# Optimization experiments

Measured on AMD Instinct MI355X. Metric: run time of the kernel, lower is better.

## Reference

```python
import jax, jax.numpy as jnp
import numpy as np

N = 10000       # num_nodes
E = 1000        # num_hyperedges
STEPS = 30      # horizon


def setup_inputs() -> dict:
    key = jax.random.key(0)
    k1, k2 = jax.random.split(key, 2)
    infected0 = jax.random.uniform(k1, (N,)) < 0.01
    x = jnp.stack([(~infected0).astype(jnp.float32),
                   infected0.astype(jnp.float32),
                   jnp.zeros((N,), jnp.float32)], axis=1)
    H = (jax.random.uniform(k2, (STEPS - 1, E, N)) < 0.001).astype(jnp.float32)
    beta = jnp.full((N,), 0.01, jnp.float32)
    gamma = jnp.full((N,), 0.038, jnp.float32)
    return {"x": x, "H": H, "beta": beta, "gamma": gamma, "steps": STEPS}


def _simulate(x, H, beta, gamma):
    n = x.shape[0]
    key0 = jax.random.key(42)

    def step(carry, H_t):
        p_prev, s_prev, key = carry
        key, k1, k2 = jax.random.split(key, 3)
        infected = s_prev[:, 1]
        # hypergraph Laplacian step: H_t.T @ (H_t @ infected)
        new_cases = beta * (H_t.T @ (H_t @ infected))
        new_rec = gamma * infected
        p = jnp.stack([p_prev[:, 0] - new_cases,
                       p_prev[:, 1] + new_cases - new_rec,
                       p_prev[:, 2] + new_rec], axis=1)
        p = jnp.clip(p, 0.0, 1.0)
        # per-node stochastic SIR state transitions (vectorized)
        u1 = jax.random.uniform(k1, (n,))
        u2 = jax.random.uniform(k2, (n,))
        was_S = s_prev[:, 0] == 1
        was_I = s_prev[:, 1] == 1
        s_to_I = was_S & (u1 < p[:, 1])
        i_event = was_I & (u1 < p[:, 2])
        i_to_R = i_event & (u2 < 0.5)
        i_to_S = i_event & ~(u2 < 0.5)
        new_S = (was_S & ~s_to_I) | i_to_S
        new_I = s_to_I | (was_I & ~i_event)
        new_R = (~was_S & ~was_I) | i_to_R
        s = jnp.stack([new_S, new_I, new_R], axis=1).astype(x.dtype)
        return (p, s, key), (p, s)

    (_, _, _), (p_seq, s_seq) = jax.lax.scan(step, (x, x, key0), H)
    pathogen = jnp.concatenate([x[None], p_seq], axis=0)    # (steps, N, 3)
    state = jnp.concatenate([x[None], s_seq], axis=0)       # (steps, N, 3)
    return pathogen, state


def reference(x, H, beta, gamma, steps):
    # steps == H.shape[0] + 1 by construction
    return _simulate(x, H, beta, gamma)
```

## Files before the change

kernel.cpp:

```cpp
#include <hip/hip_runtime.h>
#include <stdint.h>

constexpr int NN = 10000;
constexpr int EE = 1000;
constexpr int TT = 30;
constexpr int TS = TT - 1;
constexpr int ROW = NN * 3;
constexpr int S_OFF = TT * ROW;
constexpr int CAP_E = 48;
constexpr int WPR = CAP_E / 2;
constexpr int PREW = 8;
constexpr int SIMT = 1024;
constexpr int NPT  = 10;
constexpr int RBLK = (NN + SIMT - 1) / SIMT;

__host__ __device__ inline void tf2x32(uint32_t k0, uint32_t k1,
                                       uint32_t x0, uint32_t x1,
                                       uint32_t &o0, uint32_t &o1) {
  uint32_t ks2 = k0 ^ k1 ^ 0x1BD11BDAu;
  x0 += k0; x1 += k1;
#define TFR(r) do { x0 += x1; x1 = (x1 << (r)) | (x1 >> (32 - (r))); x1 ^= x0; } while (0)
  TFR(13); TFR(15); TFR(26); TFR(6);
  x0 += k1;  x1 += ks2 + 1u;
  TFR(17); TFR(29); TFR(16); TFR(24);
  x0 += ks2; x1 += k0 + 2u;
  TFR(13); TFR(15); TFR(26); TFR(6);
  x0 += k0;  x1 += k1 + 3u;
  TFR(17); TFR(29); TFR(16); TFR(24);
  x0 += k1;  x1 += ks2 + 4u;
  TFR(13); TFR(15); TFR(26); TFR(6);
  x0 += ks2; x1 += k0 + 5u;
#undef TFR
  o0 = x0; o1 = x1;
}

__device__ inline float bits_to_uniform(uint32_t bits) {
  float f = __uint_as_float((bits >> 9) | 0x3F800000u) - 1.0f;
  return f < 0.f ? 0.f : f;
}

struct StepKeys { uint32_t k1a[TS], k1b[TS], k2a[TS], k2b[TS]; };

__device__ inline void bar_lds() {
  asm volatile("s_waitcnt lgkmcnt(0)\n\ts_barrier" ::: "memory");
}

#define ALD(p)    __hip_atomic_load((p),  __ATOMIC_RELAXED, __HIP_MEMORY_SCOPE_AGENT)
#define AST(p, v) __hip_atomic_store((p), (v), __ATOMIC_RELAXED, __HIP_MEMORY_SCOPE_AGENT)

__global__ void k_zero(unsigned* __restrict__ cnt) {
  if (threadIdx.x < TS) cnt[threadIdx.x] = 0u;
}

__global__ __launch_bounds__(SIMT, 4)
void k_fused(const float* __restrict__ H,
             int* __restrict__ edge_cnt, uint32_t* __restrict__ edge_words,
             unsigned long long* __restrict__ uv, unsigned* __restrict__ cnt,
             const float* __restrict__ x,
             const float* __restrict__ beta, const float* __restrict__ gamma_,
             float* __restrict__ out, StepKeys keys) {
  const int tid = threadIdx.x;

  if (blockIdx.x > 0) {
    const int row = blockIdx.x - 1;
    const int t = row / EE;
    const int e = row - t * EE;

    if (e < RBLK) {
      int n = e * SIMT + tid;
      if (n < NN) {
        uint32_t a, b;
        tf2x32(keys.k1a[t], keys.k1b[t], 0u, (uint32_t)n, a, b);
        uint32_t b1 = __float_as_uint(bits_to_uniform(a ^ b));
        tf2x32(keys.k2a[t], keys.k2b[t], 0u, (uint32_t)n, a, b);
        uint32_t b2 = __float_as_uint(bits_to_uniform(a ^ b));
        unsigned long long raw = (unsigned long long)b1 | ((unsigned long long)b2 << 32);
        AST(&uv[(size_t)t * NN + n], raw);
      }
    }

    __shared__ int scnt;
    __shared__ uint16_t list[CAP_E];
    if (tid == 0) scnt = 0;
    __syncthreads();
    const float4* hrow = reinterpret_cast<const float4*>(H + (size_t)row * NN);
    float4 v0 = hrow[tid];
    float4 v1 = hrow[tid + 1024];
    float4 v2 = make_float4(0.f, 0.f, 0.f, 0.f);
    const bool has2 = tid + 2048 < NN / 4;
    if (has2) v2 = hrow[tid + 2048];
#define PROC(v, b4) do { \
    if ((v).x != 0.f) { int p = atomicAdd(&scnt, 1); if (p < CAP_E) list[p] = (uint16_t)((b4) + 0); } \
    if ((v).y != 0.f) { int p = atomicAdd(&scnt, 1); if (p < CAP_E) list[p] = (uint16_t)((b4) + 1); } \
    if ((v).z != 0.f) { int p = atomicAdd(&scnt, 1); if (p < CAP_E) list[p] = (uint16_t)((b4) + 2); } \
    if ((v).w != 0.f) { int p = atomicAdd(&scnt, 1); if (p < CAP_E) list[p] = (uint16_t)((b4) + 3); } \
  } while (0)
    PROC(v0, 4 * tid);
    PROC(v1, 4 * (tid + 1024));
    if (has2) PROC(v2, 4 * (tid + 2048));
#undef PROC
    __syncthreads();
    int c = scnt < CAP_E ? scnt : CAP_E;
    if (tid == 0) AST(&edge_cnt[row], c);
    int words = (c + 1) >> 1;
    int wmax = words > PREW ? words : PREW;
    if (tid < wmax) {
      uint32_t lo = (2 * tid     < c) ? (uint32_t)list[2 * tid]     : 0xFFFFu;
      uint32_t hi = (2 * tid + 1 < c) ? (uint32_t)list[2 * tid + 1] : 0xFFFFu;
      AST(&edge_words[((size_t)t * WPR + tid) * EE + e], lo | (hi << 16));
    }
    __syncthreads();
    if (tid == 0)
      __hip_atomic_fetch_add(&cnt[t], 1u, __ATOMIC_RELAXED, __HIP_MEMORY_SCOPE_AGENT);
    return;
  }

  __shared__ int nvst[NN];

  float p0[NPT], p1[NPT], p2[NPT], bet[NPT], gam[NPT];
#pragma unroll
  for (int k = 0; k < NPT; ++k) {
    int n = tid + k * SIMT;
    if (n < NN) {
      float x0 = x[n * 3 + 0], x1 = x[n * 3 + 1], x2 = x[n * 3 + 2];
      p0[k] = x0; p1[k] = x1; p2[k] = x2;
      int st = (x1 == 1.f) ? 1 : ((x0 == 1.f) ? 0 : 2);
      nvst[n] = st << 16;
      bet[k] = beta[n]; gam[k] = gamma_[n];
      out[n * 3 + 0] = x0; out[n * 3 + 1] = x1; out[n * 3 + 2] = x2;
      out[S_OFF + n * 3 + 0] = x0; out[S_OFF + n * 3 + 1] = x1; out[S_OFF + n * 3 + 2] = x2;
    }
  }
  bar_lds();

  for (int t = 0; t < TS; ++t) {
    if (tid == 0) {
      while (ALD(&cnt[t]) < (unsigned)EE) __builtin_amdgcn_s_sleep(8);
    }
    bar_lds();

    float u1r[NPT], u2r[NPT];
#pragma unroll
    for (int k = 0; k < NPT; ++k) {
      int n = tid + k * SIMT;
      if (n < NN) {
        unsigned long long raw = ALD(&uv[(size_t)t * NN + n]);
        u1r[k] = __uint_as_float((uint32_t)raw);
        u2r[k] = __uint_as_float((uint32_t)(raw >> 32));
      }
    }

    if (tid < EE) {
      const uint32_t* wb = edge_words + (size_t)t * WPR * EE + tid;
      int ec = ALD(&edge_cnt[t * EE + tid]); if (ec > CAP_E) ec = CAP_E;
      uint32_t w[PREW];
#pragma unroll
      for (int j = 0; j < PREW; ++j) w[j] = ALD(&wb[(size_t)j * EE]);
      int words = (ec + 1) >> 1;
      int s = 0;
#pragma unroll
      for (int j = 0; j < PREW; ++j) {
        uint32_t lo = w[j] & 0xFFFFu, hi = w[j] >> 16;
        if (lo != 0xFFFFu) s += ((nvst[lo] >> 16) == 1) ? 1 : 0;
        if (hi != 0xFFFFu) s += ((nvst[hi] >> 16) == 1) ? 1 : 0;
      }
      for (int j = PREW; j < words; ++j) {
        uint32_t ww = ALD(&wb[(size_t)j * EE]);
        uint32_t lo = ww & 0xFFFFu, hi = ww >> 16;
        if (lo != 0xFFFFu) s += ((nvst[lo] >> 16) == 1) ? 1 : 0;
        if (hi != 0xFFFFu) s += ((nvst[hi] >> 16) == 1) ? 1 : 0;
      }
      if (s > 0) {
#pragma unroll
        for (int j = 0; j < PREW; ++j) {
          uint32_t lo = w[j] & 0xFFFFu, hi = w[j] >> 16;
          if (lo != 0xFFFFu) atomicAdd(&nvst[lo], s);
          if (hi != 0xFFFFu) atomicAdd(&nvst[hi], s);
        }
        for (int j = PREW; j < words; ++j) {
          uint32_t ww = ALD(&wb[(size_t)j * EE]);
          uint32_t lo = ww & 0xFFFFu, hi = ww >> 16;
          if (lo != 0xFFFFu) atomicAdd(&nvst[lo], s);
          if (hi != 0xFFFFu) atomicAdd(&nvst[hi], s);
        }
      }
    }
    bar_lds();

    float* po = out + (size_t)(t + 1) * ROW;
    float* so = out + S_OFF + (size_t)(t + 1) * ROW;
#pragma unroll
    for (int k = 0; k < NPT; ++k) {
      int n = tid + k * SIMT;
      if (n < NN) {
        int wv = nvst[n];
        int v  = wv & 0xFFFF;
        int st = wv >> 16;
        float s1 = (st == 1) ? 1.f : 0.f;
        float new_cases = __fmul_rn(bet[k], (float)v);
        float new_rec   = __fmul_rn(gam[k], s1);
        float q0 = fminf(1.f, fmaxf(0.f, __fsub_rn(p0[k], new_cases)));
        float q1 = fminf(1.f, fmaxf(0.f, __fsub_rn(__fadd_rn(p1[k], new_cases), new_rec)));
        float q2 = fminf(1.f, fmaxf(0.f, __fadd_rn(p2[k], new_rec)));
        p0[k] = q0; p1[k] = q1; p2[k] = q2;

        bool was_S  = (st == 0);
        bool was_I  = (st == 1);
        bool s_to_I = was_S && (u1r[k] < q1);
        bool i_event = was_I && (u1r[k] < q2);
        bool u2lt   = (u2r[k] < 0.5f);
        bool i_to_R = i_event && u2lt;
        bool i_to_S = i_event && !u2lt;
        bool new_S = (was_S && !s_to_I) || i_to_S;
        bool new_I = s_to_I || (was_I && !i_event);
        bool new_R = (!was_S && !was_I) || i_to_R;

        po[n * 3 + 0] = q0; po[n * 3 + 1] = q1; po[n * 3 + 2] = q2;
        so[n * 3 + 0] = new_S ? 1.f : 0.f;
        so[n * 3 + 1] = new_I ? 1.f : 0.f;
        so[n * 3 + 2] = new_R ? 1.f : 0.f;
        nvst[n] = (new_I ? 1 : (new_S ? 0 : 2)) << 16;
      }
    }
  }
}

extern "C" void kernel_launch(void* const* d_in, const int* in_sizes, int n_in,
                              void* d_out, int out_size, void* d_ws, size_t ws_size,
                              hipStream_t stream) {
  const float* x      = (const float*)d_in[0];
  const float* H      = (const float*)d_in[1];
  const float* beta   = (const float*)d_in[2];
  const float* gamma_ = (const float*)d_in[3];
  float* out = (float*)d_out;

  StepKeys keys;
  uint32_t key0 = 0u, key1 = 42u;
  for (int t = 0; t < TS; ++t) {
    uint32_t a0, b0, a1, b1, a2, b2;
    tf2x32(key0, key1, 0u, 0u, a0, b0);
    tf2x32(key0, key1, 0u, 1u, a1, b1);
    tf2x32(key0, key1, 0u, 2u, a2, b2);
    keys.k1a[t] = a1; keys.k1b[t] = b1; keys.k2a[t] = a2; keys.k2b[t] = b2;
    key0 = a0; key1 = b0;
  }

  size_t off = 0;
  auto take = [&](size_t bytes) { size_t o = off; off += (bytes + 255) & ~(size_t)255; return o; };
  size_t o_ec = take((size_t)TS * EE * sizeof(int));
  size_t o_ew = take((size_t)TS * WPR * EE * sizeof(uint32_t));
  size_t o_uv = take((size_t)TS * NN * sizeof(unsigned long long));
  size_t o_ct = take((size_t)TS * sizeof(unsigned));

  int*      edge_cnt   = (int*)((char*)d_ws + o_ec);
  uint32_t* edge_words = (uint32_t*)((char*)d_ws + o_ew);
  unsigned long long* uv = (unsigned long long*)((char*)d_ws + o_uv);
  unsigned* cnt        = (unsigned*)((char*)d_ws + o_ct);

  k_zero<<<1, 64, 0, stream>>>(cnt);
  k_fused<<<1 + TS * EE, SIMT, 0, stream>>>(H, edge_cnt, edge_words, uv, cnt,
                                            x, beta, gamma_, out, keys);
}
```

Baseline: 1.608 ms.

## Process five incidence rows per producer block with upfront batched loads

Each producer block now handles five consecutive hyperedge rows of the same timestep instead of one. All five rows of H are loaded into registers before processing, which raises memory-level parallelism. It also cuts the block count and the per-block launch and sync overhead by five. RNG generation is regrouped so the same node range is still covered, and the completion counter advances by five per block. The costs are more registers per thread and LDS barriers between the serial per-row compaction passes.

```diff
diff --git a/kernel.cpp b/kernel.cpp
--- a/kernel.cpp
+++ b/kernel.cpp
@@ -13,6 +13,8 @@
 constexpr int SIMT = 1024;
 constexpr int NPT  = 10;
 constexpr int RBLK = (NN + SIMT - 1) / SIMT;
+constexpr int RPB  = 5;
+static_assert(EE % RPB == 0, "rows of a block must share one t");
 
 __host__ __device__ inline void tf2x32(uint32_t k0, uint32_t k1,
                                        uint32_t x0, uint32_t x1,
@@ -62,56 +64,71 @@
   const int tid = threadIdx.x;
 
   if (blockIdx.x > 0) {
-    const int row = blockIdx.x - 1;
-    const int t = row / EE;
-    const int e = row - t * EE;
-
-    if (e < RBLK) {
-      int n = e * SIMT + tid;
-      if (n < NN) {
-        uint32_t a, b;
-        tf2x32(keys.k1a[t], keys.k1b[t], 0u, (uint32_t)n, a, b);
-        uint32_t b1 = __float_as_uint(bits_to_uniform(a ^ b));
-        tf2x32(keys.k2a[t], keys.k2b[t], 0u, (uint32_t)n, a, b);
-        uint32_t b2 = __float_as_uint(bits_to_uniform(a ^ b));
-        unsigned long long raw = (unsigned long long)b1 | ((unsigned long long)b2 << 32);
-        AST(&uv[(size_t)t * NN + n], raw);
+    const int base  = (blockIdx.x - 1) * RPB;
+    const int t     = base / EE;
+    const int ebase = base - t * EE;
+
+    const float4* h0 = reinterpret_cast<const float4*>(H + (size_t)base * NN);
+    const bool has2 = (tid + 2048) < (NN / 4);
+    float4 v[RPB][3];
+#pragma unroll
+    for (int r = 0; r < RPB; ++r) {
+      const float4* hrow = h0 + (size_t)r * (NN / 4);
+      v[r][0] = hrow[tid];
+      v[r][1] = hrow[tid + 1024];
+      v[r][2] = has2 ? hrow[tid + 2048] : make_float4(0.f, 0.f, 0.f, 0.f);
+    }
+
+    if (ebase < RBLK) {
+#pragma unroll
+      for (int r = 0; r < RPB; ++r) {
+        int e = ebase + r;
+        int n = e * SIMT + tid;
+        if (n < NN) {
+          uint32_t a, b;
+          tf2x32(keys.k1a[t], keys.k1b[t], 0u, (uint32_t)n, a, b);
+          uint32_t b1 = __float_as_uint(bits_to_uniform(a ^ b));
+          tf2x32(keys.k2a[t], keys.k2b[t], 0u, (uint32_t)n, a, b);
+          uint32_t b2 = __float_as_uint(bits_to_uniform(a ^ b));
+          unsigned long long raw = (unsigned long long)b1 | ((unsigned long long)b2 << 32);
+          AST(&uv[(size_t)t * NN + n], raw);
+        }
       }
     }
 
     __shared__ int scnt;
     __shared__ uint16_t list[CAP_E];
-    if (tid == 0) scnt = 0;
-    __syncthreads();
-    const float4* hrow = reinterpret_cast<const float4*>(H + (size_t)row * NN);
-    float4 v0 = hrow[tid];
-    float4 v1 = hrow[tid + 1024];
-    float4 v2 = make_float4(0.f, 0.f, 0.f, 0.f);
-    const bool has2 = tid + 2048 < NN / 4;
-    if (has2) v2 = hrow[tid + 2048];
-#define PROC(v, b4) do { \
-    if ((v).x != 0.f) { int p = atomicAdd(&scnt, 1); if (p < CAP_E) list[p] = (uint16_t)((b4) + 0); } \
-    if ((v).y != 0.f) { int p = atomicAdd(&scnt, 1); if (p < CAP_E) list[p] = (uint16_t)((b4) + 1); } \
-    if ((v).z != 0.f) { int p = atomicAdd(&scnt, 1); if (p < CAP_E) list[p] = (uint16_t)((b4) + 2); } \
-    if ((v).w != 0.f) { int p = atomicAdd(&scnt, 1); if (p < CAP_E) list[p] = (uint16_t)((b4) + 3); } \
+#define PROC(vv, b4) do { \
+    if ((vv).x != 0.f) { int p = atomicAdd(&scnt, 1); if (p < CAP_E) list[p] = (uint16_t)((b4) + 0); } \
+    if ((vv).y != 0.f) { int p = atomicAdd(&scnt, 1); if (p < CAP_E) list[p] = (uint16_t)((b4) + 1); } \
+    if ((vv).z != 0.f) { int p = atomicAdd(&scnt, 1); if (p < CAP_E) list[p] = (uint16_t)((b4) + 2); } \
+    if ((vv).w != 0.f) { int p = atomicAdd(&scnt, 1); if (p < CAP_E) list[p] = (uint16_t)((b4) + 3); } \
   } while (0)
-    PROC(v0, 4 * tid);
-    PROC(v1, 4 * (tid + 1024));
-    if (has2) PROC(v2, 4 * (tid + 2048));
+
+#pragma unroll
+    for (int r = 0; r < RPB; ++r) {
+      if (r > 0) bar_lds();
+      if (tid == 0) scnt = 0;
+      bar_lds();
+      PROC(v[r][0], 4 * tid);
+      PROC(v[r][1], 4 * (tid + 1024));
+      if (has2) PROC(v[r][2], 4 * (tid + 2048));
+      bar_lds();
+      int c = scnt < CAP_E ? scnt : CAP_E;
+      const int e = ebase + r;
+      if (tid == 0) AST(&edge_cnt[t * EE + e], c);
+      int words = (c + 1) >> 1;
+      int wmax = words > PREW ? words : PREW;
+      if (tid < wmax) {
+        uint32_t lo = (2 * tid     < c) ? (uint32_t)list[2 * tid]     : 0xFFFFu;
+        uint32_t hi = (2 * tid + 1 < c) ? (uint32_t)list[2 * tid + 1] : 0xFFFFu;
+        AST(&edge_words[((size_t)t * WPR + tid) * EE + e], lo | (hi << 16));
+      }
+    }
 #undef PROC
     __syncthreads();
-    int c = scnt < CAP_E ? scnt : CAP_E;
-    if (tid == 0) AST(&edge_cnt[row], c);
-    int words = (c + 1) >> 1;
-    int wmax = words > PREW ? words : PREW;
-    if (tid < wmax) {
-      uint32_t lo = (2 * tid     < c) ? (uint32_t)list[2 * tid]     : 0xFFFFu;
-      uint32_t hi = (2 * tid + 1 < c) ? (uint32_t)list[2 * tid + 1] : 0xFFFFu;
-      AST(&edge_words[((size_t)t * WPR + tid) * EE + e], lo | (hi << 16));
-    }
-    __syncthreads();
     if (tid == 0)
-      __hip_atomic_fetch_add(&cnt[t], 1u, __ATOMIC_RELAXED, __HIP_MEMORY_SCOPE_AGENT);
+      __hip_atomic_fetch_add(&cnt[t], (unsigned)RPB, __ATOMIC_RELAXED, __HIP_MEMORY_SCOPE_AGENT);
     return;
   }
 
@@ -258,6 +275,6 @@
   unsigned* cnt        = (unsigned*)((char*)d_ws + o_ct);
 
   k_zero<<<1, 64, 0, stream>>>(cnt);
-  k_fused<<<1 + TS * EE, SIMT, 0, stream>>>(H, edge_cnt, edge_words, uv, cnt,
-                                            x, beta, gamma_, out, keys);
-}
+  k_fused<<<1 + (TS * EE) / RPB, SIMT, 0, stream>>>(H, edge_cnt, edge_words, uv, cnt,
+                                                    x, beta, gamma_, out, keys);
+}
```

Measured after the change: 1.480 ms. 8.0% less time.

## Scan one H row per wavefront with ballot compaction and register prefetch

Applied to the files above, without the earlier changes.

Producer blocks now handle 16 hyperedge rows each, one per wavefront, instead of one row per 1024-thread block. Each wave streams its row through an 8-deep float4 register prefetch ring and compacts the nonzero node indices with ballot/mbcnt instead of LDS atomics. This cuts the producer grid from about 29k blocks to about 1.8k and lets one counter atomic cover several rows. In exchange each wave issues many serial chunk loads per row, and the random-number rows are spread across fewer blocks.

```diff
diff --git a/kernel.cpp b/kernel.cpp
--- a/kernel.cpp
+++ b/kernel.cpp
@@ -13,6 +13,13 @@
 constexpr int SIMT = 1024;
 constexpr int NPT  = 10;
 constexpr int RBLK = (NN + SIMT - 1) / SIMT;
+constexpr int WAVES = SIMT / 64;
+constexpr int NROWS = TS * EE;
+constexpr int SCANB = (NROWS + WAVES - 1) / WAVES;
+constexpr int F4R   = NN / 4;
+constexpr int CHUNKS = (F4R + 63) / 64;
+constexpr int PDEPTH = 8;
+static_assert(CHUNKS % PDEPTH == 0, "rotated pipeline wants CHUNKS % PDEPTH == 0");
 
 __host__ __device__ inline void tf2x32(uint32_t k0, uint32_t k1,
                                        uint32_t x0, uint32_t x1,
@@ -55,63 +62,101 @@
 __global__ __launch_bounds__(SIMT, 4)
 void k_fused(const float* __restrict__ H,
              int* __restrict__ edge_cnt, uint32_t* __restrict__ edge_words,
-             unsigned long long* __restrict__ uv, unsigned* __restrict__ cnt,
+             unsigned long long* __restrict__ uv, unsigned* __restrict__ cntg,
              const float* __restrict__ x,
              const float* __restrict__ beta, const float* __restrict__ gamma_,
              float* __restrict__ out, StepKeys keys) {
   const int tid = threadIdx.x;
 
   if (blockIdx.x > 0) {
-    const int row = blockIdx.x - 1;
-    const int t = row / EE;
-    const int e = row - t * EE;
-
-    if (e < RBLK) {
-      int n = e * SIMT + tid;
-      if (n < NN) {
-        uint32_t a, b;
-        tf2x32(keys.k1a[t], keys.k1b[t], 0u, (uint32_t)n, a, b);
-        uint32_t b1 = __float_as_uint(bits_to_uniform(a ^ b));
-        tf2x32(keys.k2a[t], keys.k2b[t], 0u, (uint32_t)n, a, b);
-        uint32_t b2 = __float_as_uint(bits_to_uniform(a ^ b));
-        unsigned long long raw = (unsigned long long)b1 | ((unsigned long long)b2 << 32);
-        AST(&uv[(size_t)t * NN + n], raw);
-      }
-    }
-
-    __shared__ int scnt;
-    __shared__ uint16_t list[CAP_E];
-    if (tid == 0) scnt = 0;
+    const int base  = (blockIdx.x - 1) * WAVES;
+    int nrows = NROWS - base; if (nrows > WAVES) nrows = WAVES;
+    const int wid  = tid >> 6;
+    const int lane = tid & 63;
+    const int row  = base + wid;
+    const bool rvalid = wid < nrows;
+
+    __shared__ uint16_t wlist[WAVES][CAP_E];
+
+    const float4* hrow = reinterpret_cast<const float4*>(H) + (size_t)row * F4R;
+    float4 bufs[PDEPTH];
+    if (rvalid) {
+#pragma unroll
+      for (int p = 0; p < PDEPTH; ++p) bufs[p] = hrow[lane + 64 * p];
+    }
+
+    for (int r = base; r < base + nrows; ++r) {
+      int tt = r / EE;
+      int ee = r - tt * EE;
+      if (ee < RBLK) {
+        int n = ee * SIMT + tid;
+        if (n < NN) {
+          uint32_t a, b;
+          tf2x32(keys.k1a[tt], keys.k1b[tt], 0u, (uint32_t)n, a, b);
+          uint32_t b1 = __float_as_uint(bits_to_uniform(a ^ b));
+          tf2x32(keys.k2a[tt], keys.k2b[tt], 0u, (uint32_t)n, a, b);
+          uint32_t b2 = __float_as_uint(bits_to_uniform(a ^ b));
+          unsigned long long raw = (unsigned long long)b1 | ((unsigned long long)b2 << 32);
+          AST(&uv[(size_t)tt * NN + n], raw);
+        }
+      }
+    }
+
+    if (rvalid) {
+      const int t = row / EE;
+      const int e = row - t * EE;
+      uint16_t* wl = wlist[wid];
+      int lc = 0;
+
+#define PROCC(val, nodeid) do { \
+        bool nz = (val) != 0.f; \
+        unsigned long long m = __ballot(nz); \
+        int pref = __builtin_amdgcn_mbcnt_hi((unsigned)(m >> 32), \
+                     __builtin_amdgcn_mbcnt_lo((unsigned)m, 0u)); \
+        if (nz) { int pos = lc + pref; if (pos < CAP_E) wl[pos] = (uint16_t)(nodeid); } \
+        lc += __popcll(m); \
+      } while (0)
+
+      for (int c8 = 0; c8 < CHUNKS; c8 += PDEPTH) {
+#pragma unroll
+        for (int p = 0; p < PDEPTH; ++p) {
+          const int ch = c8 + p;
+          float4 v = bufs[p];
+          int nc = ch + PDEPTH;
+          if (nc < CHUNKS) {
+            int nidx = lane + 64 * nc;
+            bufs[p] = (nidx < F4R) ? hrow[nidx] : make_float4(0.f, 0.f, 0.f, 0.f);
+          }
+          int node = 4 * (lane + 64 * ch);
+          PROCC(v.x, node + 0);
+          PROCC(v.y, node + 1);
+          PROCC(v.z, node + 2);
+          PROCC(v.w, node + 3);
+        }
+      }
+#undef PROCC
+
+      int c = lc < CAP_E ? lc : CAP_E;
+      if (lane == 0) AST(&edge_cnt[row], c);
+      int words = (c + 1) >> 1;
+      int wmax = words > PREW ? words : PREW;
+      if (lane < wmax) {
+        uint32_t lo = (2 * lane     < c) ? (uint32_t)wl[2 * lane]     : 0xFFFFu;
+        uint32_t hi = (2 * lane + 1 < c) ? (uint32_t)wl[2 * lane + 1] : 0xFFFFu;
+        AST(&edge_words[((size_t)t * WPR + lane) * EE + e], lo | (hi << 16));
+      }
+    }
     __syncthreads();
-    const float4* hrow = reinterpret_cast<const float4*>(H + (size_t)row * NN);
-    float4 v0 = hrow[tid];
-    float4 v1 = hrow[tid + 1024];
-    float4 v2 = make_float4(0.f, 0.f, 0.f, 0.f);
-    const bool has2 = tid + 2048 < NN / 4;
-    if (has2) v2 = hrow[tid + 2048];
-#define PROC(v, b4) do { \
-    if ((v).x != 0.f) { int p = atomicAdd(&scnt, 1); if (p < CAP_E) list[p] = (uint16_t)((b4) + 0); } \
-    if ((v).y != 0.f) { int p = atomicAdd(&scnt, 1); if (p < CAP_E) list[p] = (uint16_t)((b4) + 1); } \
-    if ((v).z != 0.f) { int p = atomicAdd(&scnt, 1); if (p < CAP_E) list[p] = (uint16_t)((b4) + 2); } \
-    if ((v).w != 0.f) { int p = atomicAdd(&scnt, 1); if (p < CAP_E) list[p] = (uint16_t)((b4) + 3); } \
-  } while (0)
-    PROC(v0, 4 * tid);
-    PROC(v1, 4 * (tid + 1024));
-    if (has2) PROC(v2, 4 * (tid + 2048));
-#undef PROC
-    __syncthreads();
-    int c = scnt < CAP_E ? scnt : CAP_E;
-    if (tid == 0) AST(&edge_cnt[row], c);
-    int words = (c + 1) >> 1;
-    int wmax = words > PREW ? words : PREW;
-    if (tid < wmax) {
-      uint32_t lo = (2 * tid     < c) ? (uint32_t)list[2 * tid]     : 0xFFFFu;
-      uint32_t hi = (2 * tid + 1 < c) ? (uint32_t)list[2 * tid + 1] : 0xFFFFu;
-      AST(&edge_words[((size_t)t * WPR + tid) * EE + e], lo | (hi << 16));
-    }
-    __syncthreads();
-    if (tid == 0)
-      __hip_atomic_fetch_add(&cnt[t], 1u, __ATOMIC_RELAXED, __HIP_MEMORY_SCOPE_AGENT);
+    if (tid == 0) {
+      int t0 = base / EE;
+      int e0 = base - t0 * EE;
+      int in0 = EE - e0; if (in0 > nrows) in0 = nrows;
+      __hip_atomic_fetch_add(&cntg[t0], (unsigned)in0,
+                             __ATOMIC_RELAXED, __HIP_MEMORY_SCOPE_AGENT);
+      if (nrows > in0)
+        __hip_atomic_fetch_add(&cntg[t0 + 1], (unsigned)(nrows - in0),
+                               __ATOMIC_RELAXED, __HIP_MEMORY_SCOPE_AGENT);
+    }
     return;
   }
 
@@ -135,7 +180,7 @@
 
   for (int t = 0; t < TS; ++t) {
     if (tid == 0) {
-      while (ALD(&cnt[t]) < (unsigned)EE) __builtin_amdgcn_s_sleep(8);
+      while (ALD(&cntg[t]) < (unsigned)EE) __builtin_amdgcn_s_sleep(8);
     }
     bar_lds();
 
@@ -258,6 +303,6 @@
   unsigned* cnt        = (unsigned*)((char*)d_ws + o_ct);
 
   k_zero<<<1, 64, 0, stream>>>(cnt);
-  k_fused<<<1 + TS * EE, SIMT, 0, stream>>>(H, edge_cnt, edge_words, uv, cnt,
-                                            x, beta, gamma_, out, keys);
-}
+  k_fused<<<1 + SCANB, SIMT, 0, stream>>>(H, edge_cnt, edge_words, uv, cnt,
+                                          x, beta, gamma_, out, keys);
+}
```

Result: faster. 1.548 ms (-3.8%).

## Split the serial time loop into per-step blocks chained by flags, batch H scanning

Applied to the files above, without the earlier changes.

The single block that ran all 29 steps is replaced by 29 step blocks. Each step block generates its own random numbers locally and prepares its edge lists ahead of time. It then waits on a flag for the previous step's packed 2-bit node states and reads the previous probabilities from the output. The scan blocks now handle 20 H rows each, with register prefetch of upcoming rows, which cuts the block count and per-block overhead. The chain is still serial across steps, and it now adds a global handoff and a state reload per step in exchange for overlap and better occupancy. The scheme also relies on all step blocks being co-resident.

```diff
diff --git a/kernel.cpp b/kernel.cpp
--- a/kernel.cpp
+++ b/kernel.cpp
@@ -12,7 +12,13 @@
 constexpr int PREW = 8;
 constexpr int SIMT = 1024;
 constexpr int NPT  = 10;
-constexpr int RBLK = (NN + SIMT - 1) / SIMT;
+constexpr int NROWS = TS * EE;
+constexpr int F4R   = NN / 4;
+constexpr int RPB   = 20;
+constexpr int PK    = 5;
+constexpr int SCANB = NROWS / RPB;
+constexpr int PACKW = (NN + 15) / 16;
+static_assert(EE % RPB == 0 && NROWS % RPB == 0 && RPB % PK == 0, "geometry");
 
 __host__ __device__ inline void tf2x32(uint32_t k0, uint32_t k1,
                                        uint32_t x0, uint32_t x1,
@@ -45,184 +51,235 @@
   asm volatile("s_waitcnt lgkmcnt(0)\n\ts_barrier" ::: "memory");
 }
 
-#define ALD(p)    __hip_atomic_load((p),  __ATOMIC_RELAXED, __HIP_MEMORY_SCOPE_AGENT)
-#define AST(p, v) __hip_atomic_store((p), (v), __ATOMIC_RELAXED, __HIP_MEMORY_SCOPE_AGENT)
-
-__global__ void k_zero(unsigned* __restrict__ cnt) {
-  if (threadIdx.x < TS) cnt[threadIdx.x] = 0u;
+#define ALD(p)     __hip_atomic_load((p),  __ATOMIC_RELAXED, __HIP_MEMORY_SCOPE_AGENT)
+#define AST(p, v)  __hip_atomic_store((p), (v), __ATOMIC_RELAXED, __HIP_MEMORY_SCOPE_AGENT)
+
+__global__ void k_zero(unsigned* __restrict__ cnt, unsigned* __restrict__ stflag) {
+  if (threadIdx.x < TS) { cnt[threadIdx.x] = 0u; stflag[threadIdx.x] = 0u; }
 }
 
 __global__ __launch_bounds__(SIMT, 4)
 void k_fused(const float* __restrict__ H,
              int* __restrict__ edge_cnt, uint32_t* __restrict__ edge_words,
-             unsigned long long* __restrict__ uv, unsigned* __restrict__ cnt,
+             unsigned* __restrict__ stbuf, unsigned* __restrict__ stflag,
+             unsigned* __restrict__ cntg,
              const float* __restrict__ x,
              const float* __restrict__ beta, const float* __restrict__ gamma_,
              float* __restrict__ out, StepKeys keys) {
   const int tid = threadIdx.x;
-
-  if (blockIdx.x > 0) {
-    const int row = blockIdx.x - 1;
-    const int t = row / EE;
-    const int e = row - t * EE;
-
-    if (e < RBLK) {
-      int n = e * SIMT + tid;
-      if (n < NN) {
-        uint32_t a, b;
-        tf2x32(keys.k1a[t], keys.k1b[t], 0u, (uint32_t)n, a, b);
-        uint32_t b1 = __float_as_uint(bits_to_uniform(a ^ b));
-        tf2x32(keys.k2a[t], keys.k2b[t], 0u, (uint32_t)n, a, b);
-        uint32_t b2 = __float_as_uint(bits_to_uniform(a ^ b));
-        unsigned long long raw = (unsigned long long)b1 | ((unsigned long long)b2 << 32);
-        AST(&uv[(size_t)t * NN + n], raw);
-      }
-    }
-
-    __shared__ int scnt;
-    __shared__ uint16_t list[CAP_E];
-    if (tid == 0) scnt = 0;
-    __syncthreads();
-    const float4* hrow = reinterpret_cast<const float4*>(H + (size_t)row * NN);
-    float4 v0 = hrow[tid];
-    float4 v1 = hrow[tid + 1024];
-    float4 v2 = make_float4(0.f, 0.f, 0.f, 0.f);
-    const bool has2 = tid + 2048 < NN / 4;
-    if (has2) v2 = hrow[tid + 2048];
-#define PROC(v, b4) do { \
-    if ((v).x != 0.f) { int p = atomicAdd(&scnt, 1); if (p < CAP_E) list[p] = (uint16_t)((b4) + 0); } \
-    if ((v).y != 0.f) { int p = atomicAdd(&scnt, 1); if (p < CAP_E) list[p] = (uint16_t)((b4) + 1); } \
-    if ((v).z != 0.f) { int p = atomicAdd(&scnt, 1); if (p < CAP_E) list[p] = (uint16_t)((b4) + 2); } \
-    if ((v).w != 0.f) { int p = atomicAdd(&scnt, 1); if (p < CAP_E) list[p] = (uint16_t)((b4) + 3); } \
+  const int bi  = blockIdx.x;
+
+  if (bi >= TS) {
+    const int base = (bi - TS) * RPB;
+    const int t    = base / EE;
+    const int e0   = base - t * EE;
+
+    __shared__ int      scnt_arr[RPB];
+    __shared__ uint16_t lists[RPB][CAP_E];
+    if (tid < RPB) scnt_arr[tid] = 0;
+
+    const float4* h0 = reinterpret_cast<const float4*>(H) + (size_t)base * F4R;
+    const bool has2 = tid < F4R - 2048;
+
+    float4 b0[PK], b1[PK], b2[PK];
+#pragma unroll
+    for (int p = 0; p < PK; ++p) {
+      const float4* hr = h0 + (size_t)p * F4R;
+      b0[p] = hr[tid];
+      b1[p] = hr[tid + 1024];
+      b2[p] = has2 ? hr[tid + 2048] : make_float4(0.f, 0.f, 0.f, 0.f);
+    }
+    bar_lds();
+
+#define PROCS(vv, b4, rr) do { \
+    if ((vv).x != 0.f) { int q = atomicAdd(&scnt_arr[rr], 1); if (q < CAP_E) lists[rr][q] = (uint16_t)((b4) + 0); } \
+    if ((vv).y != 0.f) { int q = atomicAdd(&scnt_arr[rr], 1); if (q < CAP_E) lists[rr][q] = (uint16_t)((b4) + 1); } \
+    if ((vv).z != 0.f) { int q = atomicAdd(&scnt_arr[rr], 1); if (q < CAP_E) lists[rr][q] = (uint16_t)((b4) + 2); } \
+    if ((vv).w != 0.f) { int q = atomicAdd(&scnt_arr[rr], 1); if (q < CAP_E) lists[rr][q] = (uint16_t)((b4) + 3); } \
   } while (0)
-    PROC(v0, 4 * tid);
-    PROC(v1, 4 * (tid + 1024));
-    if (has2) PROC(v2, 4 * (tid + 2048));
-#undef PROC
-    __syncthreads();
-    int c = scnt < CAP_E ? scnt : CAP_E;
-    if (tid == 0) AST(&edge_cnt[row], c);
-    int words = (c + 1) >> 1;
-    int wmax = words > PREW ? words : PREW;
-    if (tid < wmax) {
-      uint32_t lo = (2 * tid     < c) ? (uint32_t)list[2 * tid]     : 0xFFFFu;
-      uint32_t hi = (2 * tid + 1 < c) ? (uint32_t)list[2 * tid + 1] : 0xFFFFu;
-      AST(&edge_words[((size_t)t * WPR + tid) * EE + e], lo | (hi << 16));
-    }
+
+    for (int o = 0; o < RPB / PK; ++o) {
+#pragma unroll
+      for (int p = 0; p < PK; ++p) {
+        const int r = o * PK + p;
+        float4 va = b0[p], vb = b1[p], vc = b2[p];
+        if (o + 1 < RPB / PK) {
+          const float4* hr = h0 + (size_t)(r + PK) * F4R;
+          b0[p] = hr[tid];
+          b1[p] = hr[tid + 1024];
+          if (has2) b2[p] = hr[tid + 2048];
+        }
+        PROCS(va, 4 * tid, r);
+        PROCS(vb, 4 * (tid + 1024), r);
+        if (has2) PROCS(vc, 4 * (tid + 2048), r);
+        bar_lds();
+        int c = scnt_arr[r]; c = c < CAP_E ? c : CAP_E;
+        const int row = base + r, e = e0 + r;
+        if (tid == 0) AST(&edge_cnt[row], c);
+        int words = (c + 1) >> 1;
+        int wmax = words > PREW ? words : PREW;
+        if (tid < wmax) {
+          uint32_t lo = (2 * tid     < c) ? (uint32_t)lists[r][2 * tid]     : 0xFFFFu;
+          uint32_t hi = (2 * tid + 1 < c) ? (uint32_t)lists[r][2 * tid + 1] : 0xFFFFu;
+          AST(&edge_words[((size_t)t * WPR + tid) * EE + e], lo | (hi << 16));
+        }
+      }
+    }
+#undef PROCS
     __syncthreads();
     if (tid == 0)
-      __hip_atomic_fetch_add(&cnt[t], 1u, __ATOMIC_RELAXED, __HIP_MEMORY_SCOPE_AGENT);
+      __hip_atomic_fetch_add(&cntg[t], (unsigned)RPB,
+                             __ATOMIC_RELAXED, __HIP_MEMORY_SCOPE_AGENT);
     return;
   }
 
-  __shared__ int nvst[NN];
-
-  float p0[NPT], p1[NPT], p2[NPT], bet[NPT], gam[NPT];
+  const int t = bi;
+  __shared__ int      nvst[NN];
+  __shared__ unsigned stpack[PACKW];
+
+  float u1r[NPT], u2r[NPT], bet[NPT], gam[NPT], p0a[NPT], p1a[NPT], p2a[NPT];
 #pragma unroll
   for (int k = 0; k < NPT; ++k) {
     int n = tid + k * SIMT;
     if (n < NN) {
-      float x0 = x[n * 3 + 0], x1 = x[n * 3 + 1], x2 = x[n * 3 + 2];
-      p0[k] = x0; p1[k] = x1; p2[k] = x2;
-      int st = (x1 == 1.f) ? 1 : ((x0 == 1.f) ? 0 : 2);
-      nvst[n] = st << 16;
+      uint32_t a, b;
+      tf2x32(keys.k1a[t], keys.k1b[t], 0u, (uint32_t)n, a, b);
+      u1r[k] = bits_to_uniform(a ^ b);
+      tf2x32(keys.k2a[t], keys.k2b[t], 0u, (uint32_t)n, a, b);
+      u2r[k] = bits_to_uniform(a ^ b);
       bet[k] = beta[n]; gam[k] = gamma_[n];
-      out[n * 3 + 0] = x0; out[n * 3 + 1] = x1; out[n * 3 + 2] = x2;
-      out[S_OFF + n * 3 + 0] = x0; out[S_OFF + n * 3 + 1] = x1; out[S_OFF + n * 3 + 2] = x2;
-    }
-  }
-  bar_lds();
-
-  for (int t = 0; t < TS; ++t) {
-    if (tid == 0) {
-      while (ALD(&cnt[t]) < (unsigned)EE) __builtin_amdgcn_s_sleep(8);
-    }
-    bar_lds();
-
-    float u1r[NPT], u2r[NPT];
+    }
+  }
+  if (t == 0) {
+    if (tid < PACKW) stpack[tid] = 0u;
 #pragma unroll
     for (int k = 0; k < NPT; ++k) {
       int n = tid + k * SIMT;
       if (n < NN) {
-        unsigned long long raw = ALD(&uv[(size_t)t * NN + n]);
-        u1r[k] = __uint_as_float((uint32_t)raw);
-        u2r[k] = __uint_as_float((uint32_t)(raw >> 32));
-      }
-    }
-
-    if (tid < EE) {
-      const uint32_t* wb = edge_words + (size_t)t * WPR * EE + tid;
-      int ec = ALD(&edge_cnt[t * EE + tid]); if (ec > CAP_E) ec = CAP_E;
-      uint32_t w[PREW];
-#pragma unroll
-      for (int j = 0; j < PREW; ++j) w[j] = ALD(&wb[(size_t)j * EE]);
-      int words = (ec + 1) >> 1;
-      int s = 0;
+        float x0 = x[n * 3 + 0], x1 = x[n * 3 + 1], x2 = x[n * 3 + 2];
+        p0a[k] = x0; p1a[k] = x1; p2a[k] = x2;
+        int st = (x1 == 1.f) ? 1 : ((x0 == 1.f) ? 0 : 2);
+        nvst[n] = st << 16;
+        out[n * 3 + 0] = x0; out[n * 3 + 1] = x1; out[n * 3 + 2] = x2;
+        out[S_OFF + n * 3 + 0] = x0; out[S_OFF + n * 3 + 1] = x1; out[S_OFF + n * 3 + 2] = x2;
+      }
+    }
+  }
+
+  if (tid == 0) {
+    while (ALD(&cntg[t]) < (unsigned)EE) __builtin_amdgcn_s_sleep(8);
+  }
+  bar_lds();
+  int ec = 0; uint32_t w[PREW];
+  const uint32_t* wb = edge_words + (size_t)t * WPR * EE + tid;
+  if (tid < EE) {
+    ec = ALD(&edge_cnt[t * EE + tid]); if (ec > CAP_E) ec = CAP_E;
+#pragma unroll
+    for (int j = 0; j < PREW; ++j) w[j] = ALD(&wb[(size_t)j * EE]);
+  }
+
+  if (t > 0) {
+    if (tid == 0) {
+      while (ALD(&stflag[t - 1]) == 0u) __builtin_amdgcn_s_sleep(8);
+    }
+    bar_lds();
+    const float* pp = out + (size_t)t * ROW;
+#pragma unroll
+    for (int k = 0; k < NPT; ++k) {
+      int n = tid + k * SIMT;
+      if (n < NN) {
+        p0a[k] = ALD(&pp[n * 3 + 0]);
+        p1a[k] = ALD(&pp[n * 3 + 1]);
+        p2a[k] = ALD(&pp[n * 3 + 2]);
+      }
+    }
+    if (tid < PACKW) stpack[tid] = ALD(&stbuf[(size_t)(t - 1) * PACKW + tid]);
+    bar_lds();
+#pragma unroll
+    for (int k = 0; k < NPT; ++k) {
+      int n = tid + k * SIMT;
+      if (n < NN) {
+        int st = (int)((stpack[n >> 4] >> ((n & 15) * 2)) & 3u);
+        nvst[n] = st << 16;
+      }
+    }
+    bar_lds();
+    if (tid < PACKW) stpack[tid] = 0u;
+  }
+
+  if (tid < EE) {
+    int words = (ec + 1) >> 1;
+    int s = 0;
+#pragma unroll
+    for (int j = 0; j < PREW; ++j) {
+      uint32_t lo = w[j] & 0xFFFFu, hi = w[j] >> 16;
+      if (lo != 0xFFFFu) s += ((nvst[lo] >> 16) == 1) ? 1 : 0;
+      if (hi != 0xFFFFu) s += ((nvst[hi] >> 16) == 1) ? 1 : 0;
+    }
+    for (int j = PREW; j < words; ++j) {
+      uint32_t ww = ALD(&wb[(size_t)j * EE]);
+      uint32_t lo = ww & 0xFFFFu, hi = ww >> 16;
+      if (lo != 0xFFFFu) s += ((nvst[lo] >> 16) == 1) ? 1 : 0;
+      if (hi != 0xFFFFu) s += ((nvst[hi] >> 16) == 1) ? 1 : 0;
+    }
+    if (s > 0) {
 #pragma unroll
       for (int j = 0; j < PREW; ++j) {
         uint32_t lo = w[j] & 0xFFFFu, hi = w[j] >> 16;
-        if (lo != 0xFFFFu) s += ((nvst[lo] >> 16) == 1) ? 1 : 0;
-        if (hi != 0xFFFFu) s += ((nvst[hi] >> 16) == 1) ? 1 : 0;
+        if (lo != 0xFFFFu) atomicAdd(&nvst[lo], s);
+        if (hi != 0xFFFFu) atomicAdd(&nvst[hi], s);
       }
       for (int j = PREW; j < words; ++j) {
         uint32_t ww = ALD(&wb[(size_t)j * EE]);
         uint32_t lo = ww & 0xFFFFu, hi = ww >> 16;
-        if (lo != 0xFFFFu) s += ((nvst[lo] >> 16) == 1) ? 1 : 0;
-        if (hi != 0xFFFFu) s += ((nvst[hi] >> 16) == 1) ? 1 : 0;
-      }
-      if (s > 0) {
-#pragma unroll
-        for (int j = 0; j < PREW; ++j) {
-          uint32_t lo = w[j] & 0xFFFFu, hi = w[j] >> 16;
-          if (lo != 0xFFFFu) atomicAdd(&nvst[lo], s);
-          if (hi != 0xFFFFu) atomicAdd(&nvst[hi], s);
-        }
-        for (int j = PREW; j < words; ++j) {
-          uint32_t ww = ALD(&wb[(size_t)j * EE]);
-          uint32_t lo = ww & 0xFFFFu, hi = ww >> 16;
-          if (lo != 0xFFFFu) atomicAdd(&nvst[lo], s);
-          if (hi != 0xFFFFu) atomicAdd(&nvst[hi], s);
-        }
-      }
-    }
-    bar_lds();
-
-    float* po = out + (size_t)(t + 1) * ROW;
-    float* so = out + S_OFF + (size_t)(t + 1) * ROW;
-#pragma unroll
-    for (int k = 0; k < NPT; ++k) {
-      int n = tid + k * SIMT;
-      if (n < NN) {
-        int wv = nvst[n];
-        int v  = wv & 0xFFFF;
-        int st = wv >> 16;
-        float s1 = (st == 1) ? 1.f : 0.f;
-        float new_cases = __fmul_rn(bet[k], (float)v);
-        float new_rec   = __fmul_rn(gam[k], s1);
-        float q0 = fminf(1.f, fmaxf(0.f, __fsub_rn(p0[k], new_cases)));
-        float q1 = fminf(1.f, fmaxf(0.f, __fsub_rn(__fadd_rn(p1[k], new_cases), new_rec)));
-        float q2 = fminf(1.f, fmaxf(0.f, __fadd_rn(p2[k], new_rec)));
-        p0[k] = q0; p1[k] = q1; p2[k] = q2;
-
-        bool was_S  = (st == 0);
-        bool was_I  = (st == 1);
-        bool s_to_I = was_S && (u1r[k] < q1);
-        bool i_event = was_I && (u1r[k] < q2);
-        bool u2lt   = (u2r[k] < 0.5f);
-        bool i_to_R = i_event && u2lt;
-        bool i_to_S = i_event && !u2lt;
-        bool new_S = (was_S && !s_to_I) || i_to_S;
-        bool new_I = s_to_I || (was_I && !i_event);
-        bool new_R = (!was_S && !was_I) || i_to_R;
-
-        po[n * 3 + 0] = q0; po[n * 3 + 1] = q1; po[n * 3 + 2] = q2;
-        so[n * 3 + 0] = new_S ? 1.f : 0.f;
-        so[n * 3 + 1] = new_I ? 1.f : 0.f;
-        so[n * 3 + 2] = new_R ? 1.f : 0.f;
-        nvst[n] = (new_I ? 1 : (new_S ? 0 : 2)) << 16;
-      }
-    }
-  }
+        if (lo != 0xFFFFu) atomicAdd(&nvst[lo], s);
+        if (hi != 0xFFFFu) atomicAdd(&nvst[hi], s);
+      }
+    }
+  }
+  bar_lds();
+
+  float* po = out + (size_t)(t + 1) * ROW;
+  float* so = out + S_OFF + (size_t)(t + 1) * ROW;
+#pragma unroll
+  for (int k = 0; k < NPT; ++k) {
+    int n = tid + k * SIMT;
+    if (n < NN) {
+      int wv = nvst[n];
+      int v  = wv & 0xFFFF;
+      int st = wv >> 16;
+      float s1 = (st == 1) ? 1.f : 0.f;
+      float new_cases = __fmul_rn(bet[k], (float)v);
+      float new_rec   = __fmul_rn(gam[k], s1);
+      float q0 = fminf(1.f, fmaxf(0.f, __fsub_rn(p0a[k], new_cases)));
+      float q1 = fminf(1.f, fmaxf(0.f, __fsub_rn(__fadd_rn(p1a[k], new_cases), new_rec)));
+      float q2 = fminf(1.f, fmaxf(0.f, __fadd_rn(p2a[k], new_rec)));
+
+      bool was_S  = (st == 0);
+      bool was_I  = (st == 1);
+      bool s_to_I = was_S && (u1r[k] < q1);
+      bool i_event = was_I && (u1r[k] < q2);
+      bool u2lt   = (u2r[k] < 0.5f);
+      bool i_to_R = i_event && u2lt;
+      bool i_to_S = i_event && !u2lt;
+      bool new_S = (was_S && !s_to_I) || i_to_S;
+      bool new_I = s_to_I || (was_I && !i_event);
+      bool new_R = (!was_S && !was_I) || i_to_R;
+
+      AST(&po[n * 3 + 0], q0);
+      AST(&po[n * 3 + 1], q1);
+      AST(&po[n * 3 + 2], q2);
+      so[n * 3 + 0] = new_S ? 1.f : 0.f;
+      so[n * 3 + 1] = new_I ? 1.f : 0.f;
+      so[n * 3 + 2] = new_R ? 1.f : 0.f;
+      int stn = new_I ? 1 : (new_S ? 0 : 2);
+      atomicOr(&stpack[n >> 4], (unsigned)stn << ((n & 15) * 2));
+    }
+  }
+  bar_lds();
+  if (tid < PACKW) AST(&stbuf[(size_t)t * PACKW + tid], stpack[tid]);
+  __syncthreads();
+  if (tid == 0) AST(&stflag[t], 1u);
 }
 
 extern "C" void kernel_launch(void* const* d_in, const int* in_sizes, int n_in,
@@ -249,15 +306,17 @@
   auto take = [&](size_t bytes) { size_t o = off; off += (bytes + 255) & ~(size_t)255; return o; };
   size_t o_ec = take((size_t)TS * EE * sizeof(int));
   size_t o_ew = take((size_t)TS * WPR * EE * sizeof(uint32_t));
-  size_t o_uv = take((size_t)TS * NN * sizeof(unsigned long long));
+  size_t o_sb = take((size_t)TS * PACKW * sizeof(unsigned));
   size_t o_ct = take((size_t)TS * sizeof(unsigned));
+  size_t o_fl = take((size_t)TS * sizeof(unsigned));
 
   int*      edge_cnt   = (int*)((char*)d_ws + o_ec);
   uint32_t* edge_words = (uint32_t*)((char*)d_ws + o_ew);
-  unsigned long long* uv = (unsigned long long*)((char*)d_ws + o_uv);
+  unsigned* stbuf      = (unsigned*)((char*)d_ws + o_sb);
   unsigned* cnt        = (unsigned*)((char*)d_ws + o_ct);
-
-  k_zero<<<1, 64, 0, stream>>>(cnt);
-  k_fused<<<1 + TS * EE, SIMT, 0, stream>>>(H, edge_cnt, edge_words, uv, cnt,
-                                            x, beta, gamma_, out, keys);
-}
+  unsigned* stflag     = (unsigned*)((char*)d_ws + o_fl);
+
+  k_zero<<<1, 64, 0, stream>>>(cnt, stflag);
+  k_fused<<<TS + SCANB, SIMT, 0, stream>>>(H, edge_cnt, edge_words, stbuf, stflag,
+                                           cnt, x, beta, gamma_, out, keys);
+}
```

After: 1.879 ms. +16.8%, slower.
